# Optimization experiments

Measured on AMD Instinct MI355X. Metric: run time of the kernel, lower is better.

## Reference

```python
import jax, jax.numpy as jnp
import numpy as np

MAX_CLASSES = 10
LN_EPS = 1e-5


def _g_features(L):
    # L: (B, T, k) logits -> sorted G-matrix fingerprint (B, k*(k+1)//2)
    P = jax.nn.softmax(L, axis=-1)
    T = P.shape[1]
    k = P.shape[-1]
    G = jnp.einsum('btk,btl->bkl', P, P) / T  # (B, k, k)
    diag = jnp.diagonal(G, axis1=1, axis2=2)  # (B, k)
    diag_sorted = jnp.sort(diag, axis=-1)[:, ::-1]
    iu0, iu1 = np.triu_indices(k, 1)
    off = G[:, iu0, iu1]  # (B, k*(k-1)//2)
    off_sorted = jnp.sort(off, axis=-1)[:, ::-1]
    return jnp.concatenate([diag_sorted, off_sorted], axis=-1)


def setup_inputs() -> dict:
    key = jax.random.key(0)
    ks = list(range(2, MAX_CLASSES + 1))
    keys = jax.random.split(key, len(ks) + 3)
    B, T = 256, 4096
    inp = {}
    for i, k in enumerate(ks):
        inp[f'logits_k{k}'] = jax.random.normal(keys[i], (B, T, k), dtype=jnp.float32)
    input_dim = sum(k * (k + 1) // 2 for k in ks)  # 219
    hidden = 256
    out_dim = MAX_CLASSES - 1
    inp['ln_gamma'] = jnp.ones((input_dim,), jnp.float32)
    inp['ln_beta'] = jnp.zeros((input_dim,), jnp.float32)
    inp['w1'] = jax.random.normal(keys[-3], (input_dim, hidden), jnp.float32) * 0.05
    inp['b1'] = jnp.zeros((hidden,), jnp.float32)
    inp['w2'] = jax.random.normal(keys[-2], (hidden, hidden), jnp.float32) * 0.05
    inp['b2'] = jnp.zeros((hidden,), jnp.float32)
    inp['w3'] = jax.random.normal(keys[-1], (hidden, out_dim), jnp.float32) * 0.05
    inp['b3'] = jnp.zeros((out_dim,), jnp.float32)
    return inp


def reference(logits_k2, logits_k3, logits_k4, logits_k5, logits_k6,
              logits_k7, logits_k8, logits_k9, logits_k10,
              ln_gamma, ln_beta, w1, b1, w2, b2, w3, b3):
    all_logits = [logits_k2, logits_k3, logits_k4, logits_k5, logits_k6,
                  logits_k7, logits_k8, logits_k9, logits_k10]
    feats = jnp.concatenate([_g_features(L) for L in all_logits], axis=-1)  # (B, 219)
    # LayerNorm over last dim
    mu = jnp.mean(feats, axis=-1, keepdims=True)
    var = jnp.var(feats, axis=-1, keepdims=True)
    x = (feats - mu) * jax.lax.rsqrt(var + LN_EPS) * ln_gamma + ln_beta
    # MLP (exact GELU, matching torch nn.GELU default)
    h = jax.nn.gelu(x @ w1 + b1, approximate=False)
    h = jax.nn.gelu(h @ w2 + b2, approximate=False)
    return h @ w3 + b3  # (B, max_classes-1)
```

## Files before the change

### kernel.cpp

```cpp
#include <hip/hip_runtime.h>
#include <hip/hip_bf16.h>
#include <math.h>

#define BB 256
#define TT 4096

typedef float f4 __attribute__((ext_vector_type(4)));

typedef const __attribute__((address_space(1))) void* as1_t;
typedef __attribute__((address_space(3))) void* as3_t;

__device__ __forceinline__ void gl_lds16(const float* g, const float* l) {
    __builtin_amdgcn_global_load_lds((as1_t)g, (as3_t)l, 16, 0, 0);
}

__constant__ int SEGF[10] = {0, 3, 9, 19, 34, 55, 83, 119, 164, 219};

template <int K>
__device__ __forceinline__ void row_update(float (&v)[K],
                                           float (&acc)[K * (K + 1) / 2]) {
    float m = v[0];
#pragma unroll
    for (int c = 1; c < K; ++c) m = fmaxf(m, v[c]);
    float s = 0.f;
#pragma unroll
    for (int c = 0; c < K; ++c) { v[c] = __expf(v[c] - m); s += v[c]; }
    const float inv = 1.0f / s;
#pragma unroll
    for (int c = 0; c < K; ++c) v[c] *= inv;
    int idx = 0;
#pragma unroll
    for (int i = 0; i < K; ++i) {
#pragma unroll
        for (int j = i; j < K; ++j) {
            acc[idx] = fmaf(v[i], v[j], acc[idx]);
            ++idx;
        }
    }
}

template <int K>
__device__ __forceinline__ void g_accum(const float* __restrict__ L,
                                        float* __restrict__ gdst,
                                        float* __restrict__ ldsAll,
                                        float* __restrict__ part, int b,
                                        int ch) {
    constexpr int NACC = K * (K + 1) / 2;
    const int tid = threadIdx.x;
    const int lane = tid & 63;
    const int w = tid >> 6;

    float acc[NACC];
#pragma unroll
    for (int i = 0; i < NACC; ++i) acc[i] = 0.f;

    const float* Lw = L + ((size_t)b * TT + (size_t)ch * 2048 + (size_t)w * 512) * K;

    if constexpr (K == 2 || K == 4 || K == 8) {
        constexpr int NF = (K == 8) ? 2 : 1;
        constexpr int RPF = (K == 2) ? 2 : 1;
        constexpr int TR = 64 * RPF;
        constexpr int NT = 512 / TR;
        f4 cur[NF], nxt[NF];
        {
            const float* p = Lw + (size_t)lane * 4 * NF;
#pragma unroll
            for (int f = 0; f < NF; ++f) cur[f] = *(const f4*)(p + 4 * f);
        }
#pragma unroll
        for (int t = 0; t < NT; ++t) {
            if (t < NT - 1) {
                const float* p = Lw + (size_t)(t + 1) * TR * K + (size_t)lane * 4 * NF;
#pragma unroll
                for (int f = 0; f < NF; ++f) nxt[f] = *(const f4*)(p + 4 * f);
            }
#pragma unroll
            for (int r = 0; r < RPF; ++r) {
                float v[K];
#pragma unroll
                for (int c = 0; c < K; ++c) {
                    const int fl = r * K + c;
                    v[c] = cur[fl >> 2][fl & 3];
                }
                row_update<K>(v, acc);
            }
#pragma unroll
            for (int f = 0; f < NF; ++f) cur[f] = nxt[f];
        }
    } else {
        constexpr int VF = K / 4;
        constexpr int RL = 16 * (K % 4);
        constexpr int VOPS = VF + (RL ? 1 : 0);
        float* bA = ldsAll + w * 2 * 640;
        float* bB = bA + 640;

        {
            const float* src = Lw;
#pragma unroll
            for (int s = 0; s < VF; ++s)
                gl_lds16(src + s * 256 + lane * 4, bA + s * 256);
            if constexpr (RL > 0)
                if (lane < RL) gl_lds16(src + VF * 256 + lane * 4, bA + VF * 256);
        }
#pragma unroll
        for (int t = 0; t < 8; ++t) {
            float* rd = (t & 1) ? bB : bA;
            float* wr = (t & 1) ? bA : bB;
            if (t < 7) {
                const float* src = Lw + (size_t)(t + 1) * 64 * K;
#pragma unroll
                for (int s = 0; s < VF; ++s)
                    gl_lds16(src + s * 256 + lane * 4, wr + s * 256);
                if constexpr (RL > 0)
                    if (lane < RL) gl_lds16(src + VF * 256 + lane * 4, wr + VF * 256);
                __builtin_amdgcn_s_waitcnt(0xF70 | VOPS);
            } else {
                __builtin_amdgcn_s_waitcnt(0xF70);
            }
            __builtin_amdgcn_sched_barrier(0);
            const float* myrow = rd + lane * K;
            float v[K];
#pragma unroll
            for (int c = 0; c < K; ++c) v[c] = myrow[c];
            row_update<K>(v, acc);
        }
    }

#pragma unroll
    for (int i = 0; i < NACC; ++i) {
        float x = acc[i];
#pragma unroll
        for (int off = 32; off > 0; off >>= 1) x += __shfl_down(x, off, 64);
        if (lane == 0) part[w * 55 + i] = x;
    }
    __syncthreads();

    if (tid < NACC) {
        const float x = part[0 * 55 + tid] + part[1 * 55 + tid] +
                        part[2 * 55 + tid] + part[3 * 55 + tid];
        int i = 0, rem = tid;
        while (rem >= K - i) { rem -= K - i; ++i; }
        const int j = i + rem;
        int tgt;
        if (j == i) tgt = i;
        else tgt = K + i * (K - 1) - (i * (i - 1)) / 2 + (j - i - 1);
        gdst[tgt] = x;
    }
}

__global__ __launch_bounds__(256, 3) void g_kernel(
    const float* __restrict__ l2, const float* __restrict__ l3,
    const float* __restrict__ l4, const float* __restrict__ l5,
    const float* __restrict__ l6, const float* __restrict__ l7,
    const float* __restrict__ l8, const float* __restrict__ l9,
    const float* __restrict__ l10, float* __restrict__ ws) {
    __shared__ float lds[4 * 2 * 640];
    __shared__ float part[4 * 55];
    const int flat = blockIdx.x;
    const int kslot = flat >> 9;
    const int kidx = 8 - kslot;
    const int idx = flat & 511;
    const int b = idx >> 1;
    const int ch = idx & 1;
    float* gdst = ws + ((size_t)(b * 9 + kidx) * 2 + ch) * 55;
    switch (kidx) {
        case 0: g_accum<2>(l2, gdst, lds, part, b, ch); break;
        case 1: g_accum<3>(l3, gdst, lds, part, b, ch); break;
        case 2: g_accum<4>(l4, gdst, lds, part, b, ch); break;
        case 3: g_accum<5>(l5, gdst, lds, part, b, ch); break;
        case 4: g_accum<6>(l6, gdst, lds, part, b, ch); break;
        case 5: g_accum<7>(l7, gdst, lds, part, b, ch); break;
        case 6: g_accum<8>(l8, gdst, lds, part, b, ch); break;
        case 7: g_accum<9>(l9, gdst, lds, part, b, ch); break;
        case 8: g_accum<10>(l10, gdst, lds, part, b, ch); break;
    }
}

__device__ __forceinline__ float gelu_exact(float x) {
    return 0.5f * x * (1.0f + erff(x * 0.70710678118654752440f));
}

__global__ __launch_bounds__(256) void head_kernel(
    const float* __restrict__ ws, const float* __restrict__ gamma,
    const float* __restrict__ beta, const float* __restrict__ w1,
    const float* __restrict__ b1, const float* __restrict__ w2,
    const float* __restrict__ b2, const float* __restrict__ w3,
    const float* __restrict__ b3, float* __restrict__ out) {
    const int b = blockIdx.x;
    const int tid = threadIdx.x;

    __shared__ float pre[219];
    __shared__ float srt[219];
    __shared__ float xln[219];
    __shared__ float h1[256];
    __shared__ float h2[256];
    __shared__ float rs1[4], rs2[4];
    __shared__ float smu, srv;

    if (tid < 219) {
        int ik = 0;
        while (tid >= SEGF[ik + 1]) ++ik;
        const int local = tid - SEGF[ik];
        const float* p0 = ws + ((size_t)(b * 9 + ik) * 2) * 55;
        pre[tid] = (p0[local] + p0[55 + local]) * (1.0f / (float)TT);
    }
    __syncthreads();

    if (tid < 219) {
        int ik = 0;
        while (tid >= SEGF[ik + 1]) ++ik;
        const int K = ik + 2;
        const int base = SEGF[ik];
        const int local = tid - base;
        int sstart, slen, lidx;
        if (local < K) { sstart = base; slen = K; lidx = local; }
        else { sstart = base + K; slen = (K * (K - 1)) / 2; lidx = local - K; }
        const float v = pre[tid];
        int rank = 0;
        for (int m = 0; m < slen; ++m) {
            const float u = pre[sstart + m];
            rank += (u > v) || ((u == v) && (m < lidx));
        }
        srt[sstart + rank] = v;
    }
    __syncthreads();

    const float val = (tid < 219) ? srt[tid] : 0.f;
    float s1 = val, s2 = val * val;
#pragma unroll
    for (int off = 32; off > 0; off >>= 1) {
        s1 += __shfl_down(s1, off, 64);
        s2 += __shfl_down(s2, off, 64);
    }
    const int wave = tid >> 6, lane = tid & 63;
    if (lane == 0) { rs1[wave] = s1; rs2[wave] = s2; }
    __syncthreads();
    if (tid == 0) {
        const float t1 = rs1[0] + rs1[1] + rs1[2] + rs1[3];
        const float t2 = rs2[0] + rs2[1] + rs2[2] + rs2[3];
        const float mu = t1 * (1.0f / 219.0f);
        const float var = t2 * (1.0f / 219.0f) - mu * mu;
        smu = mu;
        srv = rsqrtf(var + 1e-5f);
    }
    __syncthreads();
    if (tid < 219) xln[tid] = (srt[tid] - smu) * srv * gamma[tid] + beta[tid];
    __syncthreads();

    {
        float a = b1[tid];
#pragma unroll 8
        for (int i = 0; i < 219; ++i) a = fmaf(xln[i], w1[i * 256 + tid], a);
        h1[tid] = gelu_exact(a);
    }
    __syncthreads();

    {
        float c = b2[tid];
#pragma unroll 8
        for (int i = 0; i < 256; ++i) c = fmaf(h1[i], w2[i * 256 + tid], c);
        h2[tid] = gelu_exact(c);
    }
    __syncthreads();

    if (tid < 9) {
        float o = b3[tid];
#pragma unroll 8
        for (int i = 0; i < 256; ++i) o = fmaf(h2[i], w3[i * 9 + tid], o);
        out[(size_t)b * 9 + tid] = o;
    }
}

extern "C" void kernel_launch(void* const* d_in, const int* in_sizes, int n_in,
                              void* d_out, int out_size, void* d_ws,
                              size_t ws_size, hipStream_t stream) {
    const float* l2 = (const float*)d_in[0];
    const float* l3 = (const float*)d_in[1];
    const float* l4 = (const float*)d_in[2];
    const float* l5 = (const float*)d_in[3];
    const float* l6 = (const float*)d_in[4];
    const float* l7 = (const float*)d_in[5];
    const float* l8 = (const float*)d_in[6];
    const float* l9 = (const float*)d_in[7];
    const float* l10 = (const float*)d_in[8];
    const float* gamma = (const float*)d_in[9];
    const float* beta = (const float*)d_in[10];
    const float* w1 = (const float*)d_in[11];
    const float* b1 = (const float*)d_in[12];
    const float* w2 = (const float*)d_in[13];
    const float* b2 = (const float*)d_in[14];
    const float* w3 = (const float*)d_in[15];
    const float* b3 = (const float*)d_in[16];

    float* wsf = (float*)d_ws;
    float* outp = (float*)d_out;

    g_kernel<<<9 * 512, 256, 0, stream>>>(l2, l3, l4, l5, l6, l7, l8, l9, l10,
                                          wsf);
    head_kernel<<<BB, 256, 0, stream>>>(wsf, gamma, beta, w1, b1, w2, b2, w3,
                                        b3, outp);
}
```

Measured before the change: 100.7 us.

## Split G-accumulation into lo/hi kernels, dividing large-K accumulators across wave pairs

For k=7..10, each pair of waves now reads the same 1024-row slice, and each wave accumulates only half of the upper-triangle products. This halves per-thread accumulator registers and the FMA chain length per wave. The price is that both waves of a pair load the same rows and recompute the same softmax. Small k (2..6) moves to a separate kernel, and k=8 now uses direct vector loads with the range-restricted update. The extra launch and duplicated reads (likely served from cache) are traded for lower register pressure and shorter per-wave work on the heavy k values.

Result: slower. 136.6 us (+35.6%).

```diff
diff --git a/kernel.cpp b/kernel.cpp
--- a/kernel.cpp
+++ b/kernel.cpp
@@ -16,9 +16,9 @@
 
 __constant__ int SEGF[10] = {0, 3, 9, 19, 34, 55, 83, 119, 164, 219};
 
-template <int K>
-__device__ __forceinline__ void row_update(float (&v)[K],
-                                           float (&acc)[K * (K + 1) / 2]) {
+template <int K, int E0, int E1>
+__device__ __forceinline__ void row_update_range(float (&v)[K],
+                                                 float (&acc)[E1 - E0]) {
     float m = v[0];
 #pragma unroll
     for (int c = 1; c < K; ++c) m = fmaxf(m, v[c]);
@@ -28,23 +28,23 @@
     const float inv = 1.0f / s;
 #pragma unroll
     for (int c = 0; c < K; ++c) v[c] *= inv;
-    int idx = 0;
 #pragma unroll
     for (int i = 0; i < K; ++i) {
 #pragma unroll
         for (int j = i; j < K; ++j) {
-            acc[idx] = fmaf(v[i], v[j], acc[idx]);
-            ++idx;
+            const int idx = i * K - (i * (i - 1)) / 2 + (j - i);
+            if (idx >= E0 && idx < E1)
+                acc[idx - E0] = fmaf(v[i], v[j], acc[idx - E0]);
         }
     }
 }
 
 template <int K>
-__device__ __forceinline__ void g_accum(const float* __restrict__ L,
-                                        float* __restrict__ gdst,
-                                        float* __restrict__ ldsAll,
-                                        float* __restrict__ part, int b,
-                                        int ch) {
+__device__ __forceinline__ void g_accum_lo(const float* __restrict__ L,
+                                           float* __restrict__ gdst,
+                                           float* __restrict__ ldsAll,
+                                           float* __restrict__ part, int b,
+                                           int ch) {
     constexpr int NACC = K * (K + 1) / 2;
     const int tid = threadIdx.x;
     const int lane = tid & 63;
@@ -56,36 +56,27 @@
 
     const float* Lw = L + ((size_t)b * TT + (size_t)ch * 2048 + (size_t)w * 512) * K;
 
-    if constexpr (K == 2 || K == 4 || K == 8) {
-        constexpr int NF = (K == 8) ? 2 : 1;
+    if constexpr (K == 2 || K == 4) {
         constexpr int RPF = (K == 2) ? 2 : 1;
         constexpr int TR = 64 * RPF;
         constexpr int NT = 512 / TR;
-        f4 cur[NF], nxt[NF];
-        {
-            const float* p = Lw + (size_t)lane * 4 * NF;
-#pragma unroll
-            for (int f = 0; f < NF; ++f) cur[f] = *(const f4*)(p + 4 * f);
-        }
+        f4 cur, nxt;
+        cur = *(const f4*)(Lw + (size_t)lane * 4);
 #pragma unroll
         for (int t = 0; t < NT; ++t) {
-            if (t < NT - 1) {
-                const float* p = Lw + (size_t)(t + 1) * TR * K + (size_t)lane * 4 * NF;
-#pragma unroll
-                for (int f = 0; f < NF; ++f) nxt[f] = *(const f4*)(p + 4 * f);
+            if (t < NT - 1)
+                nxt = *(const f4*)(Lw + (size_t)(t + 1) * TR * K + (size_t)lane * 4);
+            if constexpr (K == 2) {
+#pragma unroll
+                for (int r = 0; r < 2; ++r) {
+                    float v[2] = {cur[2 * r], cur[2 * r + 1]};
+                    row_update_range<2, 0, 3>(v, acc);
+                }
+            } else {
+                float v[4] = {cur[0], cur[1], cur[2], cur[3]};
+                row_update_range<4, 0, 10>(v, acc);
             }
-#pragma unroll
-            for (int r = 0; r < RPF; ++r) {
-                float v[K];
-#pragma unroll
-                for (int c = 0; c < K; ++c) {
-                    const int fl = r * K + c;
-                    v[c] = cur[fl >> 2][fl & 3];
-                }
-                row_update<K>(v, acc);
-            }
-#pragma unroll
-            for (int f = 0; f < NF; ++f) cur[f] = nxt[f];
+            cur = nxt;
         }
     } else {
         constexpr int VF = K / 4;
@@ -93,7 +84,6 @@
         constexpr int VOPS = VF + (RL ? 1 : 0);
         float* bA = ldsAll + w * 2 * 640;
         float* bB = bA + 640;
-
         {
             const float* src = Lw;
 #pragma unroll
@@ -122,7 +112,7 @@
             float v[K];
 #pragma unroll
             for (int c = 0; c < K; ++c) v[c] = myrow[c];
-            row_update<K>(v, acc);
+            row_update_range<K, 0, NACC>(v, acc);
         }
     }
 
@@ -148,12 +138,147 @@
     }
 }
 
-__global__ __launch_bounds__(256, 3) void g_kernel(
+__global__ __launch_bounds__(256, 3) void g_lo_kernel(
     const float* __restrict__ l2, const float* __restrict__ l3,
     const float* __restrict__ l4, const float* __restrict__ l5,
-    const float* __restrict__ l6, const float* __restrict__ l7,
-    const float* __restrict__ l8, const float* __restrict__ l9,
-    const float* __restrict__ l10, float* __restrict__ ws) {
+    const float* __restrict__ l6, float* __restrict__ ws) {
+    __shared__ float lds[4 * 2 * 640];
+    __shared__ float part[4 * 55];
+    const int flat = blockIdx.x;
+    const int kslot = flat >> 9;
+    const int kidx = 4 - kslot;
+    const int idx = flat & 511;
+    const int b = idx >> 1;
+    const int ch = idx & 1;
+    float* gdst = ws + ((size_t)(b * 9 + kidx) * 2 + ch) * 55;
+    switch (kidx) {
+        case 0: g_accum_lo<2>(l2, gdst, lds, part, b, ch); break;
+        case 1: g_accum_lo<3>(l3, gdst, lds, part, b, ch); break;
+        case 2: g_accum_lo<4>(l4, gdst, lds, part, b, ch); break;
+        case 3: g_accum_lo<5>(l5, gdst, lds, part, b, ch); break;
+        case 4: g_accum_lo<6>(l6, gdst, lds, part, b, ch); break;
+    }
+}
+
+template <int K, int E0, int E1>
+__device__ __forceinline__ void g_accum_hi(const float* __restrict__ L,
+                                           float* __restrict__ ldsAll,
+                                           float* __restrict__ part, int b,
+                                           int ch) {
+    constexpr int NE = E1 - E0;
+    const int tid = threadIdx.x;
+    const int lane = tid & 63;
+    const int w = tid >> 6;
+    const int p = w >> 1;
+
+    float acc[NE];
+#pragma unroll
+    for (int i = 0; i < NE; ++i) acc[i] = 0.f;
+
+    const float* Lw = L + ((size_t)b * TT + (size_t)ch * 2048 + (size_t)p * 1024) * K;
+
+    if constexpr (K == 8) {
+        f4 cur[2], nxt[2];
+        {
+            const float* q = Lw + (size_t)lane * 8;
+            cur[0] = *(const f4*)(q);
+            cur[1] = *(const f4*)(q + 4);
+        }
+#pragma unroll
+        for (int t = 0; t < 16; ++t) {
+            if (t < 15) {
+                const float* q = Lw + (size_t)(t + 1) * 512 + (size_t)lane * 8;
+                nxt[0] = *(const f4*)(q);
+                nxt[1] = *(const f4*)(q + 4);
+            }
+            float v[8];
+#pragma unroll
+            for (int j = 0; j < 4; ++j) {
+                v[j] = cur[0][j];
+                v[4 + j] = cur[1][j];
+            }
+            row_update_range<8, E0, E1>(v, acc);
+            cur[0] = nxt[0];
+            cur[1] = nxt[1];
+        }
+    } else {
+        constexpr int VF = K / 4;
+        constexpr int RL = 16 * (K % 4);
+        constexpr int VOPS = VF + (RL ? 1 : 0);
+        float* bA = ldsAll + w * 2 * 640;
+        float* bB = bA + 640;
+        {
+            const float* src = Lw;
+#pragma unroll
+            for (int s = 0; s < VF; ++s)
+                gl_lds16(src + s * 256 + lane * 4, bA + s * 256);
+            if constexpr (RL > 0)
+                if (lane < RL) gl_lds16(src + VF * 256 + lane * 4, bA + VF * 256);
+        }
+#pragma unroll
+        for (int t = 0; t < 16; ++t) {
+            float* rd = (t & 1) ? bB : bA;
+            float* wr = (t & 1) ? bA : bB;
+            if (t < 15) {
+                const float* src = Lw + (size_t)(t + 1) * 64 * K;
+#pragma unroll
+                for (int s = 0; s < VF; ++s)
+                    gl_lds16(src + s * 256 + lane * 4, wr + s * 256);
+                if constexpr (RL > 0)
+                    if (lane < RL) gl_lds16(src + VF * 256 + lane * 4, wr + VF * 256);
+                __builtin_amdgcn_s_waitcnt(0xF70 | VOPS);
+            } else {
+                __builtin_amdgcn_s_waitcnt(0xF70);
+            }
+            __builtin_amdgcn_sched_barrier(0);
+            const float* myrow = rd + lane * K;
+            float v[K];
+#pragma unroll
+            for (int c = 0; c < K; ++c) v[c] = myrow[c];
+            row_update_range<K, E0, E1>(v, acc);
+        }
+    }
+
+#pragma unroll
+    for (int i = 0; i < NE; ++i) {
+        float x = acc[i];
+#pragma unroll
+        for (int off = 32; off > 0; off >>= 1) x += __shfl_down(x, off, 64);
+        if (lane == 0) part[w * 55 + E0 + i] = x;
+    }
+}
+
+template <int K>
+__device__ __forceinline__ void g_hi_dispatch(const float* __restrict__ L,
+                                              float* __restrict__ gdst,
+                                              float* __restrict__ ldsAll,
+                                              float* __restrict__ part, int b,
+                                              int ch) {
+    constexpr int NACC = K * (K + 1) / 2;
+    constexpr int H = (NACC + 1) / 2;
+    const int tid = threadIdx.x;
+    const int h = (tid >> 6) & 1;
+    if (h == 0) g_accum_hi<K, 0, H>(L, ldsAll, part, b, ch);
+    else        g_accum_hi<K, H, NACC>(L, ldsAll, part, b, ch);
+    __syncthreads();
+
+    if (tid < NACC) {
+        const int he = (tid >= H) ? 1 : 0;
+        const float x = part[he * 55 + tid] + part[(2 + he) * 55 + tid];
+        int i = 0, rem = tid;
+        while (rem >= K - i) { rem -= K - i; ++i; }
+        const int j = i + rem;
+        int tgt;
+        if (j == i) tgt = i;
+        else tgt = K + i * (K - 1) - (i * (i - 1)) / 2 + (j - i - 1);
+        gdst[tgt] = x;
+    }
+}
+
+__global__ __launch_bounds__(256, 3) void g_hi_kernel(
+    const float* __restrict__ l7, const float* __restrict__ l8,
+    const float* __restrict__ l9, const float* __restrict__ l10,
+    float* __restrict__ ws) {
     __shared__ float lds[4 * 2 * 640];
     __shared__ float part[4 * 55];
     const int flat = blockIdx.x;
@@ -164,15 +289,10 @@
     const int ch = idx & 1;
     float* gdst = ws + ((size_t)(b * 9 + kidx) * 2 + ch) * 55;
     switch (kidx) {
-        case 0: g_accum<2>(l2, gdst, lds, part, b, ch); break;
-        case 1: g_accum<3>(l3, gdst, lds, part, b, ch); break;
-        case 2: g_accum<4>(l4, gdst, lds, part, b, ch); break;
-        case 3: g_accum<5>(l5, gdst, lds, part, b, ch); break;
-        case 4: g_accum<6>(l6, gdst, lds, part, b, ch); break;
-        case 5: g_accum<7>(l7, gdst, lds, part, b, ch); break;
-        case 6: g_accum<8>(l8, gdst, lds, part, b, ch); break;
-        case 7: g_accum<9>(l9, gdst, lds, part, b, ch); break;
-        case 8: g_accum<10>(l10, gdst, lds, part, b, ch); break;
+        case 5: g_hi_dispatch<7>(l7, gdst, lds, part, b, ch); break;
+        case 6: g_hi_dispatch<8>(l8, gdst, lds, part, b, ch); break;
+        case 7: g_hi_dispatch<9>(l9, gdst, lds, part, b, ch); break;
+        case 8: g_hi_dispatch<10>(l10, gdst, lds, part, b, ch); break;
     }
 }
 
@@ -295,8 +415,8 @@
     float* wsf = (float*)d_ws;
     float* outp = (float*)d_out;
 
-    g_kernel<<<9 * 512, 256, 0, stream>>>(l2, l3, l4, l5, l6, l7, l8, l9, l10,
-                                          wsf);
+    g_hi_kernel<<<4 * 512, 256, 0, stream>>>(l7, l8, l9, l10, wsf);
+    g_lo_kernel<<<5 * 512, 256, 0, stream>>>(l2, l3, l4, l5, l6, wsf);
     head_kernel<<<BB, 256, 0, stream>>>(wsf, gamma, beta, w1, b1, w2, b2, w3,
                                         b3, outp);
 }
```
